# Kernel tuning notes

Hardware: AMD Instinct MI355X
Metric: run time of the kernel (lower is better)

The kernel has to match this reference:

```python
import jax, jax.numpy as jnp
import numpy as np
from jax import lax

B, T = 64, 1000
DEC, ENC, ATT, FILT, KS = 1024, 512, 128, 32, 31
PAD = (KS - 1) // 2


def setup_inputs() -> dict:
    key = jax.random.key(0)
    ks = jax.random.split(key, 9)
    return {
        "decoder_hidden": jax.random.normal(ks[0], (B, DEC), dtype=jnp.float32),
        "encoder_outputs": jax.random.normal(ks[1], (B, T, ENC), dtype=jnp.float32),
        "prev_weights": jax.random.uniform(ks[2], (B, T), dtype=jnp.float32),
        "prev_weights_cum": jax.random.uniform(ks[3], (B, T), dtype=jnp.float32),
        "mask": jnp.zeros((B, T), dtype=bool),
        # learned parameters (torch Linear weight layout: [out, in])
        "conv_w": jax.random.normal(ks[4], (FILT, 2, KS), dtype=jnp.float32) * 0.05,
        "loc_proj_w": jax.random.normal(ks[5], (ATT, FILT), dtype=jnp.float32) * 0.05,
        "query_w": jax.random.normal(ks[6], (ATT, DEC), dtype=jnp.float32) * 0.02,
        "key_w": jax.random.normal(ks[7], (ATT, ENC), dtype=jnp.float32) * 0.02,
        "value_w": jax.random.normal(ks[8], (1, ATT), dtype=jnp.float32) * 0.05,
    }


def reference(decoder_hidden, encoder_outputs, prev_weights, prev_weights_cum,
              mask, conv_w, loc_proj_w, query_w, key_w, value_w):
    # query: (B, ATT)
    query = decoder_hidden @ query_w.T
    # keys: (B, T, ATT)
    keys = jnp.einsum('bte,ae->bta', encoder_outputs, key_w)
    # location features: (B, 2, T) -> conv -> (B, FILT, T)
    loc_feats = jnp.stack([prev_weights, prev_weights_cum], axis=1)
    proc_loc = lax.conv_general_dilated(
        loc_feats, conv_w, window_strides=(1,), padding=[(PAD, PAD)],
        dimension_numbers=('NCH', 'OIH', 'NCH'))
    # (B, T, FILT) -> (B, T, ATT)
    proc_loc = jnp.einsum('bft,af->bta', proc_loc, loc_proj_w)
    # energies: (B, T)
    hidden = jnp.tanh(query[:, None, :] + keys + proc_loc)
    energies = jnp.einsum('bta,a->bt', hidden, value_w[0])
    energies = jnp.where(mask, -jnp.inf, energies)
    attention_weights = jax.nn.softmax(energies, axis=1)
    # context: (B, ENC)
    context = jnp.einsum('bt,bte->be', attention_weights, encoder_outputs)
    return context, attention_weights
```

## Files before the change

### kernel.cpp

```cpp
#include <hip/hip_runtime.h>
#include <hip/hip_bf16.h>
#include <math.h>

#define BB   64
#define TT   1000
#define DEC  1024
#define ENCD 512
#define ATT  128
#define FILT 32
#define KSZ  31
#define PADW 15
#define BT   64
#define KC   64
#define XWN  96

typedef __attribute__((ext_vector_type(8))) short bf16x8;
typedef __attribute__((ext_vector_type(4))) float f32x4;

static __device__ __forceinline__ ushort f2bf(float f) {
    union { float f; unsigned u; } v; v.f = f;
    unsigned r = (v.u + 0x7FFFu + ((v.u >> 16) & 1u)) >> 16;
    return (ushort)r;
}

static __device__ __forceinline__ bf16x8 cvt8(float4 lo, float4 hi) {
    union { __hip_bfloat162 h[4]; bf16x8 v; } u;
    u.h[0] = __float22bfloat162_rn(make_float2(lo.x, lo.y));
    u.h[1] = __float22bfloat162_rn(make_float2(lo.z, lo.w));
    u.h[2] = __float22bfloat162_rn(make_float2(hi.x, hi.y));
    u.h[3] = __float22bfloat162_rn(make_float2(hi.z, hi.w));
    return u.v;
}

static __device__ __forceinline__ float fast_tanh(float x) {
    float e = __expf(2.f * x);
    return 1.f - 2.f * __builtin_amdgcn_rcpf(e + 1.f);
}

static __device__ __forceinline__ void gl2lds16(const void* g, void* l) {
    __builtin_amdgcn_global_load_lds(
        (const __attribute__((address_space(1))) unsigned*)g,
        (__attribute__((address_space(3))) unsigned*)l, 16, 0, 0);
}

__global__ __launch_bounds__(256) void k_prep(const float* __restrict__ kw,
                                              const float* __restrict__ cw,
                                              const float* __restrict__ lpw,
                                              const float* __restrict__ dh,
                                              const float* __restrict__ qw,
                                              const float* __restrict__ vw,
                                              ushort* __restrict__ kwbF,
                                              float* __restrict__ q,
                                              float* __restrict__ Mbuf) {
    __shared__ float qred[128];
    if (blockIdx.x < 32) {
        int idx = blockIdx.x * 256 + threadIdx.x;
        int l  = idx & 63;
        int n  = (idx >> 6) & 7;
        int ks = (idx >> 9) & 1;
        int c  = idx >> 10;
        int a  = n * 16 + (l & 15);
        int k0 = c * 64 + ks * 32 + (l >> 4) * 8;
        ushort u[8];
        #pragma unroll
        for (int j = 0; j < 8; ++j) u[j] = f2bf(kw[a * ENCD + k0 + j]);
        *(uint4*)&kwbF[(size_t)idx * 8] = *(const uint4*)u;
    } else if (blockIdx.x < 36) {
        int idx = (blockIdx.x - 32) * 256 + threadIdx.x;
        int l  = idx & 63;
        int n  = (idx >> 6) & 7;
        int ks = (idx >> 9) & 1;
        int a  = n * 16 + (l & 15);
        int s  = l >> 4;
        ushort u[8];
        #pragma unroll
        for (int j = 0; j < 8; ++j) {
            int k = s * 8 + j;
            float v = 0.f;
            if (k < KSZ) {
                #pragma unroll
                for (int f = 0; f < FILT; ++f)
                    v += cw[(f * 2 + ks) * KSZ + k] * lpw[a * FILT + f];
            }
            u[j] = f2bf(v);
        }
        *(uint4*)&kwbF[(size_t)(((16 + ks) * 8 + n) * 64 + l) * 8] = *(const uint4*)u;
    } else if (blockIdx.x == 36) {
        if (threadIdx.x < 64) {
            float m0 = fabsf(vw[threadIdx.x]) + fabsf(vw[threadIdx.x + 64]);
            #pragma unroll
            for (int off = 1; off < 64; off <<= 1) m0 += __shfl_xor(m0, off, 64);
            if (threadIdx.x == 0) Mbuf[0] = m0;
        }
    } else {
        int b  = blockIdx.x - 37;
        int a  = threadIdx.x & 127;
        int kh = threadIdx.x >> 7;
        const float* dhb = dh + b * DEC + kh * 512;
        const float* qwa = qw + a * DEC + kh * 512;
        float s = 0.f;
        #pragma unroll 4
        for (int k = 0; k < 512; k += 4) {
            float4 x = *(const float4*)&dhb[k];
            float4 w = *(const float4*)&qwa[k];
            s += x.x * w.x + x.y * w.y + x.z * w.z + x.w * w.w;
        }
        if (kh == 1) qred[a] = s;
        __syncthreads();
        if (kh == 0) q[b * ATT + a] = s + qred[a];
    }
}

__global__ __launch_bounds__(256) void k_energies(
    const float* __restrict__ enc, const float* __restrict__ pw,
    const float* __restrict__ pwc, const unsigned char* __restrict__ mask,
    const ushort* __restrict__ kwbF, const float* __restrict__ vw,
    const float* __restrict__ q, const float* __restrict__ Mbuf,
    float* __restrict__ expE)
{
    __shared__ __align__(16) float Ab[BT * 64];
    __shared__ __align__(16) float xw[2][XWN];
    __shared__ float pehalf[2][BT];

    const int b   = blockIdx.x;
    const int t0  = blockIdx.y * BT;
    const int tid = threadIdx.x;
    const int w   = tid >> 6;
    const int l   = tid & 63;
    const int r   = l & 15;
    const int sl  = l >> 4;
    const int wt  = w & 1;
    const int wa  = w >> 1;

    const float* encb = enc + (size_t)b * TT * ENCD;

    const int c4src = (l & 15) ^ (w * 4 + (l >> 4));
    const float* aSrc[4];
    #pragma unroll
    for (int j = 0; j < 4; ++j) {
        int rw  = (j * 4 + w) * 4 + (l >> 4);
        int tg  = t0 + rw; if (tg >= TT) tg = TT - 1;
        aSrc[j] = encb + (size_t)tg * ENCD + c4src * 4;
    }

    for (int i = tid; i < 2 * XWN; i += 256) {
        int c  = i / XWN;
        int ii = i - c * XWN;
        int tg = t0 + ii - PADW;
        const float* src = c ? pwc : pw;
        xw[c][ii] = (ii < BT + KSZ - 1 && tg >= 0 && tg < TT) ? src[b * TT + tg] : 0.f;
    }

    f32x4 acc[2][4];
    #pragma unroll
    for (int i = 0; i < 2; ++i)
        #pragma unroll
        for (int n = 0; n < 4; ++n) acc[i][n] = (f32x4){0.f, 0.f, 0.f, 0.f};

    for (int c = 0; c < 9; ++c) {
        __syncthreads();
        if (c < 8) {
            #pragma unroll
            for (int j = 0; j < 4; ++j)
                gl2lds16(aSrc[j] + c * KC, (char*)Ab + (j * 4 + w) * 1024);
        }
        uint4 bfr[2][4];
        #pragma unroll
        for (int ks = 0; ks < 2; ++ks)
            #pragma unroll
            for (int nn = 0; nn < 4; ++nn)
                bfr[ks][nn] = *(const uint4*)&kwbF[(size_t)(((c * 2 + ks) * 8 + wa * 4 + nn) * 64 + l) * 8];
        __syncthreads();

        #pragma unroll
        for (int ks = 0; ks < 2; ++ks) {
            const int s2 = 2 * (ks * 4 + sl);
            bf16x8 af[2];
            #pragma unroll
            for (int i = 0; i < 2; ++i) {
                int row = wt * 32 + i * 16 + r;
                if (c < 8) {
                    const char* base = (const char*)Ab + row * 256;
                    float4 alo = *(const float4*)(base + ((s2 ^ r) << 4));
                    float4 ahi = *(const float4*)(base + (((s2 | 1) ^ r) << 4));
                    af[i] = cvt8(alo, ahi);
                } else {
                    const float* xp = &xw[ks][row + sl * 8];
                    float4 alo = make_float4(xp[0], xp[1], xp[2], xp[3]);
                    float4 ahi = make_float4(xp[4], xp[5], xp[6], xp[7]);
                    af[i] = cvt8(alo, ahi);
                }
            }
            #pragma unroll
            for (int i = 0; i < 2; ++i)
                #pragma unroll
                for (int nn = 0; nn < 4; ++nn)
                    acc[i][nn] = __builtin_amdgcn_mfma_f32_16x16x32_bf16(
                        af[i], *(const bf16x8*)&bfr[ks][nn], acc[i][nn], 0, 0, 0);
        }
    }

    const float* qb = q + b * ATT;
    const float M = Mbuf[0];
    float pe[2][4];
    #pragma unroll
    for (int i = 0; i < 2; ++i)
        #pragma unroll
        for (int rr = 0; rr < 4; ++rr) pe[i][rr] = 0.f;
    #pragma unroll
    for (int nn = 0; nn < 4; ++nn) {
        int a = wa * 64 + nn * 16 + r;
        float vvn = vw[a];
        float qvn = qb[a];
        #pragma unroll
        for (int i = 0; i < 2; ++i)
            #pragma unroll
            for (int rr = 0; rr < 4; ++rr)
                pe[i][rr] += vvn * fast_tanh(acc[i][nn][rr] + qvn);
    }
    #pragma unroll
    for (int m = 1; m < 16; m <<= 1)
        #pragma unroll
        for (int i = 0; i < 2; ++i)
            #pragma unroll
            for (int rr = 0; rr < 4; ++rr)
                pe[i][rr] += __shfl_xor(pe[i][rr], m, 64);
    if (r == 0) {
        #pragma unroll
        for (int i = 0; i < 2; ++i)
            #pragma unroll
            for (int rr = 0; rr < 4; ++rr)
                pehalf[wa][wt * 32 + i * 16 + sl * 4 + rr] = pe[i][rr];
    }
    __syncthreads();
    if (tid < BT) {
        int t = t0 + tid;
        if (t < TT) {
            float e = pehalf[0][tid] + pehalf[1][tid];
            float v = mask[b * TT + t] ? 0.f : __expf(e - M);
            expE[b * TT + t] = v;
        }
    }
}

#define TCH 125
__global__ __launch_bounds__(512) void k_ctx_partial(const float* __restrict__ enc,
                                                     const float* __restrict__ expE,
                                                     float* __restrict__ pctx,
                                                     float* __restrict__ ps) {
    int b = blockIdx.x, c = blockIdx.y;
    int e4 = threadIdx.x & 127;
    int g  = threadIdx.x >> 7;
    __shared__ float sw[TCH];
    int tstart = c * TCH;
    if (threadIdx.x < TCH) sw[threadIdx.x] = expE[b * TT + tstart + threadIdx.x];
    __syncthreads();
    const float* p = enc + ((size_t)b * TT + tstart) * ENCD;
    float4 acc = make_float4(0.f, 0.f, 0.f, 0.f);
    float sacc = 0.f;
    for (int t = g; t < TCH; t += 4) {
        float s = sw[t];
        float4 v = *(const float4*)(p + (size_t)t * ENCD + e4 * 4);
        acc.x += s * v.x; acc.y += s * v.y; acc.z += s * v.z; acc.w += s * v.w;
        sacc += s;
    }
    int slot = (b * 8 + c) * 4 + g;
    *(float4*)&pctx[(size_t)slot * ENCD + e4 * 4] = acc;
    if (e4 == 0) ps[slot] = sacc;
}

__global__ __launch_bounds__(512) void k_ctx_reduce(const float* __restrict__ pctx,
                                                    const float* __restrict__ ps,
                                                    const float* __restrict__ expE,
                                                    float* __restrict__ ctx,
                                                    float* __restrict__ wout) {
    int b = blockIdx.x, tid = threadIdx.x;
    __shared__ float sps[32];
    if (tid < 32) sps[tid] = ps[b * 32 + tid];
    __syncthreads();
    float s = 0.f;
    #pragma unroll
    for (int i = 0; i < 32; ++i) s += sps[i];
    float inv = 1.f / s;
    float a = 0.f;
    #pragma unroll
    for (int i = 0; i < 32; ++i) a += pctx[(size_t)(b * 32 + i) * ENCD + tid];
    ctx[b * ENCD + tid] = a * inv;
    for (int t = tid; t < TT; t += 512)
        wout[b * TT + t] = expE[b * TT + t] * inv;
}

extern "C" void kernel_launch(void* const* d_in, const int* in_sizes, int n_in,
                              void* d_out, int out_size, void* d_ws, size_t ws_size,
                              hipStream_t stream) {
    const float* dh   = (const float*)d_in[0];
    const float* enc  = (const float*)d_in[1];
    const float* pw   = (const float*)d_in[2];
    const float* pwc  = (const float*)d_in[3];
    const unsigned char* mask = (const unsigned char*)d_in[4];
    const float* cw   = (const float*)d_in[5];
    const float* lpw  = (const float*)d_in[6];
    const float* qw   = (const float*)d_in[7];
    const float* kw   = (const float*)d_in[8];
    const float* vw   = (const float*)d_in[9];

    float* out_ctx = (float*)d_out;
    float* out_w   = out_ctx + BB * ENCD;

    float* wsf    = (float*)d_ws;
    float*  q     = wsf;
    float*  expE  = wsf + 8192;
    float*  ps    = wsf + 8192 + 64000;
    float*  pctx  = wsf + 8192 + 64000 + 2048;
    ushort* kwbF  = (ushort*)(wsf + 8192 + 64000 + 2048 + 65536);
    float*  Mbuf  = wsf + 8192 + 64000 + 2048 + 65536 + 36864;

    k_prep    <<<dim3(101),    dim3(256), 0, stream>>>(kw, cw, lpw, dh, qw, vw, kwbF, q, Mbuf);
    k_energies<<<dim3(BB, 16), dim3(256), 0, stream>>>(enc, pw, pwc, mask, kwbF, vw, q, Mbuf, expE);
    k_ctx_partial<<<dim3(BB, 8), dim3(512), 0, stream>>>(enc, expE, pctx, ps);
    k_ctx_reduce <<<dim3(BB),    dim3(512), 0, stream>>>(pctx, ps, expE, out_ctx, out_w);
}
```

Baseline: 75.67 us.

## Fuse context partial sums into energies kernel and double-buffer A tiles

The partial context reduction now runs inside the energies kernel. Each block reuses its 64-row encoder tile, which is likely still in L2, to compute a weighted partial context and a partial exp sum, and the separate k_ctx_partial launch is gone. The K-loop also double-buffers the LDS A tile and the B fragments, using explicit vmcnt waits and barriers so the next chunk's loads overlap with the current MFMAs. The cost is more LDS per block, a larger workspace for the partial contexts, and a serial 64-step context loop per block that may lengthen the kernel's tail.

```diff
diff --git a/kernel.cpp b/kernel.cpp
--- a/kernel.cpp
+++ b/kernel.cpp
@@ -116,21 +116,24 @@
     const float* __restrict__ pwc, const unsigned char* __restrict__ mask,
     const ushort* __restrict__ kwbF, const float* __restrict__ vw,
     const float* __restrict__ q, const float* __restrict__ Mbuf,
-    float* __restrict__ expE)
+    float* __restrict__ expE, float* __restrict__ pctx,
+    float* __restrict__ ps)
 {
-    __shared__ __align__(16) float Ab[BT * 64];
+    __shared__ __align__(16) float Ab[2][BT * 64];
     __shared__ __align__(16) float xw[2][XWN];
     __shared__ float pehalf[2][BT];
-
-    const int b   = blockIdx.x;
-    const int t0  = blockIdx.y * BT;
-    const int tid = threadIdx.x;
-    const int w   = tid >> 6;
-    const int l   = tid & 63;
-    const int r   = l & 15;
-    const int sl  = l >> 4;
-    const int wt  = w & 1;
-    const int wa  = w >> 1;
+    __shared__ float sExp[BT];
+
+    const int b    = blockIdx.x;
+    const int tile = blockIdx.y;
+    const int t0   = tile * BT;
+    const int tid  = threadIdx.x;
+    const int w    = tid >> 6;
+    const int l    = tid & 63;
+    const int r    = l & 15;
+    const int sl   = l >> 4;
+    const int wt   = w & 1;
+    const int wa   = w >> 1;
 
     const float* encb = enc + (size_t)b * TT * ENCD;
 
@@ -151,27 +154,27 @@
         xw[c][ii] = (ii < BT + KSZ - 1 && tg >= 0 && tg < TT) ? src[b * TT + tg] : 0.f;
     }
 
+    uint4 bfr0[2][4], bfr1[2][4];
+    auto loadB = [&](uint4 (&dst)[2][4], int c) {
+        #pragma unroll
+        for (int ks = 0; ks < 2; ++ks)
+            #pragma unroll
+            for (int nn = 0; nn < 4; ++nn)
+                dst[ks][nn] = *(const uint4*)&kwbF[(size_t)(((c * 2 + ks) * 8 + wa * 4 + nn) * 64 + l) * 8];
+    };
+    auto issueA = [&](int c, int buf) {
+        #pragma unroll
+        for (int j = 0; j < 4; ++j)
+            gl2lds16(aSrc[j] + c * KC, (char*)Ab[buf] + (j * 4 + w) * 1024);
+    };
+
     f32x4 acc[2][4];
     #pragma unroll
     for (int i = 0; i < 2; ++i)
         #pragma unroll
         for (int n = 0; n < 4; ++n) acc[i][n] = (f32x4){0.f, 0.f, 0.f, 0.f};
 
-    for (int c = 0; c < 9; ++c) {
-        __syncthreads();
-        if (c < 8) {
-            #pragma unroll
-            for (int j = 0; j < 4; ++j)
-                gl2lds16(aSrc[j] + c * KC, (char*)Ab + (j * 4 + w) * 1024);
-        }
-        uint4 bfr[2][4];
-        #pragma unroll
-        for (int ks = 0; ks < 2; ++ks)
-            #pragma unroll
-            for (int nn = 0; nn < 4; ++nn)
-                bfr[ks][nn] = *(const uint4*)&kwbF[(size_t)(((c * 2 + ks) * 8 + wa * 4 + nn) * 64 + l) * 8];
-        __syncthreads();
-
+    auto compute = [&](int c, const uint4 (&bfr)[2][4]) {
         #pragma unroll
         for (int ks = 0; ks < 2; ++ks) {
             const int s2 = 2 * (ks * 4 + sl);
@@ -180,7 +183,7 @@
             for (int i = 0; i < 2; ++i) {
                 int row = wt * 32 + i * 16 + r;
                 if (c < 8) {
-                    const char* base = (const char*)Ab + row * 256;
+                    const char* base = (const char*)Ab[c & 1] + row * 256;
                     float4 alo = *(const float4*)(base + ((s2 ^ r) << 4));
                     float4 ahi = *(const float4*)(base + (((s2 | 1) ^ r) << 4));
                     af[i] = cvt8(alo, ahi);
@@ -198,6 +201,30 @@
                     acc[i][nn] = __builtin_amdgcn_mfma_f32_16x16x32_bf16(
                         af[i], *(const bf16x8*)&bfr[ks][nn], acc[i][nn], 0, 0, 0);
         }
+    };
+
+    issueA(0, 0); loadB(bfr0, 0);
+    issueA(1, 1); loadB(bfr1, 1);
+    asm volatile("s_waitcnt vmcnt(12) lgkmcnt(0)" ::: "memory");
+    __builtin_amdgcn_sched_barrier(0);
+    __builtin_amdgcn_s_barrier();
+
+    #pragma unroll
+    for (int c = 0; c < 9; ++c) {
+        if (c & 1) compute(c, bfr1); else compute(c, bfr0);
+        if (c == 8) break;
+        __builtin_amdgcn_s_barrier();
+        __builtin_amdgcn_sched_barrier(0);
+        if (c + 2 <= 8) {
+            if (c + 2 <= 7) issueA(c + 2, c & 1);
+            if (c & 1) loadB(bfr1, c + 2); else loadB(bfr0, c + 2);
+        }
+        if (c <= 4)      asm volatile("s_waitcnt vmcnt(12)" ::: "memory");
+        else if (c == 5) asm volatile("s_waitcnt vmcnt(12)" ::: "memory");
+        else if (c == 6) asm volatile("s_waitcnt vmcnt(8)"  ::: "memory");
+        else             asm volatile("s_waitcnt vmcnt(0)"  ::: "memory");
+        __builtin_amdgcn_sched_barrier(0);
+        __builtin_amdgcn_s_barrier();
     }
 
     const float* qb = q + b * ATT;
@@ -235,38 +262,27 @@
     __syncthreads();
     if (tid < BT) {
         int t = t0 + tid;
-        if (t < TT) {
-            float e = pehalf[0][tid] + pehalf[1][tid];
-            float v = mask[b * TT + t] ? 0.f : __expf(e - M);
-            expE[b * TT + t] = v;
-        }
-    }
-}
-
-#define TCH 125
-__global__ __launch_bounds__(512) void k_ctx_partial(const float* __restrict__ enc,
-                                                     const float* __restrict__ expE,
-                                                     float* __restrict__ pctx,
-                                                     float* __restrict__ ps) {
-    int b = blockIdx.x, c = blockIdx.y;
-    int e4 = threadIdx.x & 127;
-    int g  = threadIdx.x >> 7;
-    __shared__ float sw[TCH];
-    int tstart = c * TCH;
-    if (threadIdx.x < TCH) sw[threadIdx.x] = expE[b * TT + tstart + threadIdx.x];
+        float e = pehalf[0][tid] + pehalf[1][tid];
+        float v = 0.f;
+        if (t < TT && !mask[b * TT + t]) v = __expf(e - M);
+        if (t < TT) expE[b * TT + t] = v;
+        sExp[tid] = v;
+        float sv = v;
+        #pragma unroll
+        for (int off = 1; off < 64; off <<= 1) sv += __shfl_xor(sv, off, 64);
+        if (tid == 0) ps[b * 16 + tile] = sv;
+    }
     __syncthreads();
-    const float* p = enc + ((size_t)b * TT + tstart) * ENCD;
-    float4 acc = make_float4(0.f, 0.f, 0.f, 0.f);
-    float sacc = 0.f;
-    for (int t = g; t < TCH; t += 4) {
-        float s = sw[t];
-        float4 v = *(const float4*)(p + (size_t)t * ENCD + e4 * 4);
-        acc.x += s * v.x; acc.y += s * v.y; acc.z += s * v.z; acc.w += s * v.w;
-        sacc += s;
-    }
-    int slot = (b * 8 + c) * 4 + g;
-    *(float4*)&pctx[(size_t)slot * ENCD + e4 * 4] = acc;
-    if (e4 == 0) ps[slot] = sacc;
+
+    const int tmax = (TT - t0 < BT) ? (TT - t0) : BT;
+    float2 cacc = make_float2(0.f, 0.f);
+    const float* pbase = encb + (size_t)t0 * ENCD + tid * 2;
+    for (int t = 0; t < tmax; ++t) {
+        float s = sExp[t];
+        float2 v = *(const float2*)(pbase + (size_t)t * ENCD);
+        cacc.x += s * v.x; cacc.y += s * v.y;
+    }
+    *(float2*)&pctx[(size_t)(b * 16 + tile) * ENCD + tid * 2] = cacc;
 }
 
 __global__ __launch_bounds__(512) void k_ctx_reduce(const float* __restrict__ pctx,
@@ -275,16 +291,16 @@
                                                     float* __restrict__ ctx,
                                                     float* __restrict__ wout) {
     int b = blockIdx.x, tid = threadIdx.x;
-    __shared__ float sps[32];
-    if (tid < 32) sps[tid] = ps[b * 32 + tid];
+    __shared__ float sps[16];
+    if (tid < 16) sps[tid] = ps[b * 16 + tid];
     __syncthreads();
     float s = 0.f;
     #pragma unroll
-    for (int i = 0; i < 32; ++i) s += sps[i];
+    for (int i = 0; i < 16; ++i) s += sps[i];
     float inv = 1.f / s;
     float a = 0.f;
     #pragma unroll
-    for (int i = 0; i < 32; ++i) a += pctx[(size_t)(b * 32 + i) * ENCD + tid];
+    for (int i = 0; i < 16; ++i) a += pctx[(size_t)(b * 16 + i) * ENCD + tid];
     ctx[b * ENCD + tid] = a * inv;
     for (int t = tid; t < TT; t += 512)
         wout[b * TT + t] = expE[b * TT + t] * inv;
@@ -311,12 +327,11 @@
     float*  q     = wsf;
     float*  expE  = wsf + 8192;
     float*  ps    = wsf + 8192 + 64000;
-    float*  pctx  = wsf + 8192 + 64000 + 2048;
-    ushort* kwbF  = (ushort*)(wsf + 8192 + 64000 + 2048 + 65536);
-    float*  Mbuf  = wsf + 8192 + 64000 + 2048 + 65536 + 36864;
+    float*  pctx  = wsf + 8192 + 64000 + 1024;
+    ushort* kwbF  = (ushort*)(wsf + 8192 + 64000 + 1024 + 524288);
+    float*  Mbuf  = wsf + 8192 + 64000 + 1024 + 524288 + 36864;
 
     k_prep    <<<dim3(101),    dim3(256), 0, stream>>>(kw, cw, lpw, dh, qw, vw, kwbF, q, Mbuf);
-    k_energies<<<dim3(BB, 16), dim3(256), 0, stream>>>(enc, pw, pwc, mask, kwbF, vw, q, Mbuf, expE);
-    k_ctx_partial<<<dim3(BB, 8), dim3(512), 0, stream>>>(enc, expE, pctx, ps);
-    k_ctx_reduce <<<dim3(BB),    dim3(512), 0, stream>>>(pctx, ps, expE, out_ctx, out_w);
-}
+    k_energies<<<dim3(BB, 16), dim3(256), 0, stream>>>(enc, pw, pwc, mask, kwbF, vw, q, Mbuf, expE, pctx, ps);
+    k_ctx_reduce <<<dim3(BB),  dim3(512), 0, stream>>>(pctx, ps, expE, out_ctx, out_w);
+}
```

Result: faster. 67.25 us (-11.1%).
